# Optimization experiments

Measured on AMD Instinct MI355X. Metric: run time of the kernel, lower is better.

## Reference

```python
import jax, jax.numpy as jnp
import numpy as np

N, E = 50000, 600000
IN_DIM, HID, OUT = 512, 256, 64
NEG_SLOPE = 0.2  # pyg GATConv default negative_slope


def setup_inputs() -> dict:
    key = jax.random.key(0)
    ks = jax.random.split(key, 6)
    features = jax.random.normal(ks[0], (N, IN_DIM), jnp.float32)
    edge_index = jax.random.randint(ks[1], (2, E), 0, N)
    W1 = jax.random.normal(ks[2], (IN_DIM, HID), jnp.float32) * (1.0 / np.sqrt(IN_DIM))
    W2 = jax.random.normal(ks[3], (HID, OUT), jnp.float32) * (1.0 / np.sqrt(HID))
    att_src = jax.random.normal(ks[4], (HID,), jnp.float32) * 0.1
    att_dst = jax.random.normal(ks[5], (HID,), jnp.float32) * 0.1
    return {"features": features, "W1": W1, "W2": W2,
            "att_src": att_src, "att_dst": att_dst, "edge_index": edge_index}


def _gat_propagate(h_pre, a_src, a_dst, src, dst, n):
    """STAGATE GATConv message passing (heads=1, concat=False, no self loops).

    Per-edge logit = leaky_relu(alpha_src[src] + alpha_dst[dst]),
    softmax over edges sharing the same dst, scatter-add of weighted src feats.
    """
    logits = jax.nn.leaky_relu(a_src[src] + a_dst[dst], NEG_SLOPE)        # [E]
    m = jax.ops.segment_max(logits, dst, num_segments=n)                   # [N]
    ex = jnp.exp(logits - m[dst])                                          # [E]
    denom = jax.ops.segment_sum(ex, dst, num_segments=n)                   # [N]
    w = ex / (denom[dst] + 1e-16)                                          # [E], pyg softmax eps
    return jax.ops.segment_sum(h_pre[src] * w[:, None], dst, num_segments=n)  # [N, C]


def reference(features, W1, W2, att_src, att_dst, edge_index):
    src, dst = edge_index[0], edge_index[1]
    n = features.shape[0]
    # conv1: attention computed and cached (self.attentions)
    hp1 = features @ W1                      # [N, HID]
    a_s = hp1 @ att_src                      # [N] per-node src attention score
    a_d = hp1 @ att_dst                      # [N] per-node dst attention score
    h1 = jax.nn.elu(_gat_propagate(hp1, a_s, a_d, src, dst, n))
    # conv2: attention=False -> plain linear
    h2 = h1 @ W2                             # [N, OUT]
    # conv3: weights = conv2.lin_src.T, tied_attention = conv1.attentions
    hp3 = h2 @ W2.T                          # [N, HID]
    h3 = jax.nn.elu(_gat_propagate(hp3, a_s, a_d, src, dst, n))
    # conv4: weights = conv1.lin_src.T, attention=False
    h4 = h3 @ W1.T                           # [N, IN_DIM]
    return (h2, h4)
```

## Files before the change

kernel.cpp:

```cpp
#include <hip/hip_runtime.h>
#include <hip/hip_bf16.h>
#include <cstdint>
#include <cstddef>

#define IN_DIM 512
#define HID 256
#define OUTD 64
#define NEG_SLOPE 0.2f

typedef __attribute__((ext_vector_type(8))) __bf16 bfrag_t;
typedef __attribute__((ext_vector_type(4))) float facc_t;
typedef __attribute__((ext_vector_type(4))) unsigned int u32x4;

__device__ __forceinline__ float bf2f(unsigned short u) {
  return __uint_as_float(((unsigned int)u) << 16);
}
__device__ __forceinline__ unsigned short f2bf(float f) {
  unsigned int x = __float_as_uint(f);
  x = (x + 0x7FFFu + ((x >> 16) & 1u)) >> 16;
  return (unsigned short)x;
}

#define GLOAD_LDS16(g, l)                                              \
  __builtin_amdgcn_global_load_lds(                                    \
      (const __attribute__((address_space(1))) void*)(g),              \
      (__attribute__((address_space(3))) void*)(l), 16, 0, 0)

template <int BM, int BN>
__global__ __launch_bounds__(256) void gemm_bt(const unsigned short* __restrict__ A,
                                               const unsigned short* __restrict__ B,
                                               void* __restrict__ Craw,
                                               unsigned short* __restrict__ Cb,
                                               int M, int N, int K, int c32, int act) {
  constexpr int FM = BM / 32, FN = BN / 32;
  constexpr int RT = BM + BN;
  __shared__ __align__(16) unsigned short lds[RT * 32];

  const int bm0 = blockIdx.x * BM;
  const int bn0 = blockIdx.y * BN;
  const int tid = threadIdx.x;
  const int lane = tid & 63;
  const int wave = tid >> 6;
  const int wrow = (wave >> 1) * (BM / 2);
  const int wcol = (wave & 1) * (BN / 2);
  const int lr = lane & 15;
  const int quad = lane >> 4;
  const int swz = (quad ^ (lr & 3)) << 3;

  facc_t acc[FM][FN];
#pragma unroll
  for (int i = 0; i < FM; ++i)
#pragma unroll
    for (int j = 0; j < FN; ++j) acc[i][j] = (facc_t){0.f, 0.f, 0.f, 0.f};

  for (int k0 = 0; k0 < K; k0 += 32) {
    __syncthreads();
#pragma unroll
    for (int t = wave; t < RT / 16; t += 4) {
      const int r0 = t * 16;
      const int row = r0 + (lane >> 2);
      const int seg = (lane & 3) ^ (row & 3);
      const unsigned short* g;
      if (r0 < BM) {
        int gm = bm0 + row;
        if (gm >= M) gm = M - 1;
        g = A + (size_t)gm * K + k0 + seg * 8;
      } else {
        g = B + (size_t)(bn0 + row - BM) * K + k0 + seg * 8;
      }
      GLOAD_LDS16(g, lds + t * 512);
    }
    __syncthreads();

    bfrag_t a[FM], b[FN];
#pragma unroll
    for (int i = 0; i < FM; ++i)
      a[i] = *(const bfrag_t*)&lds[(wrow + i * 16 + lr) * 32 + swz];
#pragma unroll
    for (int j = 0; j < FN; ++j)
      b[j] = *(const bfrag_t*)&lds[(BM + wcol + j * 16 + lr) * 32 + swz];
#pragma unroll
    for (int i = 0; i < FM; ++i)
#pragma unroll
      for (int j = 0; j < FN; ++j)
        acc[i][j] = __builtin_amdgcn_mfma_f32_16x16x32_bf16(a[i], b[j], acc[i][j], 0, 0, 0);
  }

#pragma unroll
  for (int i = 0; i < FM; ++i)
#pragma unroll
    for (int r = 0; r < 4; ++r) {
      const int grow = bm0 + wrow + i * 16 + quad * 4 + r;
      if (grow < M) {
#pragma unroll
        for (int j = 0; j < FN; ++j) {
          const int gcol = bn0 + wcol + j * 16 + lr;
          float v = acc[i][j][r];
          if (act) v = v > 0.f ? v : (expf(v) - 1.f);
          if (c32) ((float*)Craw)[(size_t)grow * N + gcol] = v;
          else ((unsigned short*)Craw)[(size_t)grow * N + gcol] = f2bf(v);
          if (Cb) Cb[(size_t)grow * N + gcol] = f2bf(v);
        }
      }
    }
}

template <int BM, int BN>
__global__ __launch_bounds__(256) void gemm_a32_bt(const float* __restrict__ A,
                                                   const unsigned short* __restrict__ B,
                                                   unsigned short* __restrict__ C,
                                                   int M, int N, int K) {
  constexpr int FM = BM / 32, FN = BN / 32;
  constexpr int RT = BM + BN;
  __shared__ __align__(16) unsigned short lds[RT * 32];

  const int bm0 = blockIdx.x * BM;
  const int bn0 = blockIdx.y * BN;
  const int tid = threadIdx.x;
  const int lane = tid & 63;
  const int wave = tid >> 6;
  const int wrow = (wave >> 1) * (BM / 2);
  const int wcol = (wave & 1) * (BN / 2);
  const int lr = lane & 15;
  const int quad = lane >> 4;
  const int swz = (quad ^ (lr & 3)) << 3;

  const int arow0 = tid >> 2;
  const int aseg = tid & 3;

  facc_t acc[FM][FN];
#pragma unroll
  for (int i = 0; i < FM; ++i)
#pragma unroll
    for (int j = 0; j < FN; ++j) acc[i][j] = (facc_t){0.f, 0.f, 0.f, 0.f};

  for (int k0 = 0; k0 < K; k0 += 32) {
    __syncthreads();
#pragma unroll
    for (int t = wave; t < BN / 16; t += 4) {
      const int lr0 = BM + t * 16;
      const int row = lr0 + (lane >> 2);
      const int seg = (lane & 3) ^ (row & 3);
      const unsigned short* g = B + (size_t)(bn0 + t * 16 + (lane >> 2)) * K + k0 + seg * 8;
      GLOAD_LDS16(g, lds + lr0 * 32);
    }
#pragma unroll
    for (int h = 0; h < 2; ++h) {
      const int row = arow0 + h * (BM / 2);
      int gm = bm0 + row;
      if (gm >= M) gm = M - 1;
      const float* g = A + (size_t)gm * K + k0 + aseg * 8;
      const float4 fa = ((const float4*)g)[0];
      const float4 fb = ((const float4*)g)[1];
      u32x4 pk;
      pk.x = (unsigned int)f2bf(fa.x) | ((unsigned int)f2bf(fa.y) << 16);
      pk.y = (unsigned int)f2bf(fa.z) | ((unsigned int)f2bf(fa.w) << 16);
      pk.z = (unsigned int)f2bf(fb.x) | ((unsigned int)f2bf(fb.y) << 16);
      pk.w = (unsigned int)f2bf(fb.z) | ((unsigned int)f2bf(fb.w) << 16);
      *(u32x4*)&lds[row * 32 + ((aseg ^ (row & 3)) << 3)] = pk;
    }
    __syncthreads();

    bfrag_t a[FM], b[FN];
#pragma unroll
    for (int i = 0; i < FM; ++i)
      a[i] = *(const bfrag_t*)&lds[(wrow + i * 16 + lr) * 32 + swz];
#pragma unroll
    for (int j = 0; j < FN; ++j)
      b[j] = *(const bfrag_t*)&lds[(BM + wcol + j * 16 + lr) * 32 + swz];
#pragma unroll
    for (int i = 0; i < FM; ++i)
#pragma unroll
      for (int j = 0; j < FN; ++j)
        acc[i][j] = __builtin_amdgcn_mfma_f32_16x16x32_bf16(a[i], b[j], acc[i][j], 0, 0, 0);
  }

#pragma unroll
  for (int i = 0; i < FM; ++i)
#pragma unroll
    for (int r = 0; r < 4; ++r) {
      const int grow = bm0 + wrow + i * 16 + quad * 4 + r;
      if (grow < M) {
#pragma unroll
        for (int j = 0; j < FN; ++j) {
          const int gcol = bn0 + wcol + j * 16 + lr;
          C[(size_t)grow * N + gcol] = f2bf(acc[i][j][r]);
        }
      }
    }
}

__global__ void cvt_weights(const float* __restrict__ W1, const float* __restrict__ W2,
                            unsigned short* __restrict__ W1T, unsigned short* __restrict__ W1b,
                            unsigned short* __restrict__ W2T, unsigned short* __restrict__ W2b) {
  const int idx = blockIdx.x * 256 + threadIdx.x;
  if (idx < IN_DIM * HID) {
    const unsigned short b = f2bf(W1[idx]);
    W1b[idx] = b;
    const int r = idx >> 8, c = idx & 255;
    W1T[(size_t)c * IN_DIM + r] = b;
  }
  if (idx < HID * OUTD) {
    const unsigned short b = f2bf(W2[idx]);
    W2b[idx] = b;
    const int r = idx >> 6, c = idx & 63;
    W2T[(size_t)c * HID + r] = b;
  }
}

__global__ __launch_bounds__(256) void rowdot(const unsigned short* __restrict__ hp,
                                              const float* __restrict__ att_s,
                                              const float* __restrict__ att_d,
                                              float* __restrict__ as_, float* __restrict__ ad_,
                                              int n) {
  const int node = blockIdx.x * 4 + (threadIdx.x >> 6);
  if (node >= n) return;
  const int lane = threadIdx.x & 63;
  const unsigned short* row = hp + (size_t)node * HID + (lane << 2);
  float s = 0.f, d = 0.f;
#pragma unroll
  for (int j = 0; j < 4; ++j) {
    const float h = bf2f(row[j]);
    s += h * att_s[(lane << 2) + j];
    d += h * att_d[(lane << 2) + j];
  }
  for (int off = 32; off > 0; off >>= 1) {
    s += __shfl_down(s, off);
    d += __shfl_down(d, off);
  }
  if (lane == 0) { as_[node] = s; ad_[node] = d; }
}

__global__ void init_deg(int* __restrict__ deg, int n) {
  const int i = blockIdx.x * 256 + threadIdx.x;
  if (i < n) deg[i] = 0;
}

__global__ void edge_pass1(const int* __restrict__ src, const int* __restrict__ dst,
                           const float* __restrict__ as_, const float* __restrict__ ad_,
                           float* __restrict__ eexp, int* __restrict__ deg, int E, int n) {
  const int e = blockIdx.x * 256 + threadIdx.x;
  if (e >= E) return;
  const int s = src[e], d = dst[e];
  if ((unsigned)s >= (unsigned)n || (unsigned)d >= (unsigned)n) return;
  float l = as_[s] + ad_[d];
  l = l > 0.f ? l : NEG_SLOPE * l;
  eexp[e] = expf(fminf(l, 60.f));
  atomicAdd(&deg[d], 1);
}

__global__ __launch_bounds__(256) void scan_reduce(const int* __restrict__ deg,
                                                   int* __restrict__ bsum, int n) {
  __shared__ int ws4[4];
  const int tid = threadIdx.x, lane = tid & 63, wid = tid >> 6;
  const int base = blockIdx.x * 2048 + tid * 8;
  int s = 0;
#pragma unroll
  for (int j = 0; j < 8; ++j) {
    const int i = base + j;
    if (i < n) s += deg[i];
  }
  for (int off = 32; off > 0; off >>= 1) s += __shfl_down(s, off);
  if (lane == 0) ws4[wid] = s;
  __syncthreads();
  if (tid == 0) bsum[blockIdx.x] = ws4[0] + ws4[1] + ws4[2] + ws4[3];
}

__global__ __launch_bounds__(256) void scan_final(const int* __restrict__ deg,
                                                  const int* __restrict__ bsum,
                                                  int* __restrict__ row_ptr,
                                                  int* __restrict__ cursor, int n) {
  __shared__ int wsum[4];
  __shared__ int blockoff;
  const int tid = threadIdx.x, lane = tid & 63, wid = tid >> 6;
  if (wid == 0) {
    int v = (lane < blockIdx.x) ? bsum[lane] : 0;
    for (int off = 32; off > 0; off >>= 1) v += __shfl_down(v, off);
    if (lane == 0) blockoff = v;
  }
  const int base = blockIdx.x * 2048 + tid * 8;
  int v[8], s = 0;
#pragma unroll
  for (int j = 0; j < 8; ++j) {
    const int i = base + j;
    v[j] = (i < n) ? deg[i] : 0;
    s += v[j];
  }
  int ws = s;
  for (int off = 1; off < 64; off <<= 1) {
    const int t = __shfl_up(ws, off);
    if (lane >= off) ws += t;
  }
  if (lane == 63) wsum[wid] = ws;
  __syncthreads();
  int woff = 0;
  for (int w_ = 0; w_ < wid; ++w_) woff += wsum[w_];
  int run = blockoff + woff + (ws - s);
#pragma unroll
  for (int j = 0; j < 8; ++j) {
    const int i = base + j;
    if (i < n) {
      cursor[i] = run;
      row_ptr[i + 1] = run + v[j];
    }
    run += v[j];
  }
  if (blockIdx.x == 0 && tid == 0) row_ptr[0] = 0;
}

__global__ void edge_scatter(const int* __restrict__ src, const int* __restrict__ dst,
                             const float* __restrict__ eexp, int* __restrict__ cursor,
                             int2* __restrict__ csr, int E, int n) {
  const int e = blockIdx.x * 256 + threadIdx.x;
  if (e >= E) return;
  const int s = src[e], d = dst[e];
  if ((unsigned)s >= (unsigned)n || (unsigned)d >= (unsigned)n) return;
  const int pos = atomicAdd(&cursor[d], 1);
  int2 c;
  c.x = s;
  c.y = __float_as_int(eexp[e]);
  csr[pos] = c;
}

__global__ __launch_bounds__(256) void gat_prop256(const unsigned short* __restrict__ hpre,
                                                   const int* __restrict__ row_ptr,
                                                   const int2* __restrict__ csr,
                                                   unsigned short* __restrict__ out, int n) {
  const int node = blockIdx.x * 4 + (threadIdx.x >> 6);
  if (node >= n) return;
  const int lane = threadIdx.x & 63;
  const int half = lane >> 5;
  const int lh = lane & 31;
  const int beg = row_ptr[node], end = row_ptr[node + 1];
  const unsigned short* base = hpre + (lh << 3);
  float a[8] = {0.f, 0.f, 0.f, 0.f, 0.f, 0.f, 0.f, 0.f};
  float wsum = 0.f;
  int e = beg;
  for (; e + 8 <= end; e += 8) {
#pragma unroll
    for (int u = 0; u < 4; ++u) {
      const int2 c = csr[e + 2 * u + half];
      const float w = __int_as_float(c.y);
      const u32x4 v = *(const u32x4*)(base + (size_t)c.x * HID);
      wsum += w;
      a[0] += w * bf2f((unsigned short)(v.x & 0xffffu));
      a[1] += w * bf2f((unsigned short)(v.x >> 16));
      a[2] += w * bf2f((unsigned short)(v.y & 0xffffu));
      a[3] += w * bf2f((unsigned short)(v.y >> 16));
      a[4] += w * bf2f((unsigned short)(v.z & 0xffffu));
      a[5] += w * bf2f((unsigned short)(v.z >> 16));
      a[6] += w * bf2f((unsigned short)(v.w & 0xffffu));
      a[7] += w * bf2f((unsigned short)(v.w >> 16));
    }
  }
  for (; e < end; e += 2) {
    const int e2 = e + half;
    if (e2 < end) {
      const int2 c = csr[e2];
      const float w = __int_as_float(c.y);
      const u32x4 v = *(const u32x4*)(base + (size_t)c.x * HID);
      wsum += w;
      a[0] += w * bf2f((unsigned short)(v.x & 0xffffu));
      a[1] += w * bf2f((unsigned short)(v.x >> 16));
      a[2] += w * bf2f((unsigned short)(v.y & 0xffffu));
      a[3] += w * bf2f((unsigned short)(v.y >> 16));
      a[4] += w * bf2f((unsigned short)(v.z & 0xffffu));
      a[5] += w * bf2f((unsigned short)(v.z >> 16));
      a[6] += w * bf2f((unsigned short)(v.w & 0xffffu));
      a[7] += w * bf2f((unsigned short)(v.w >> 16));
    }
  }
#pragma unroll
  for (int i = 0; i < 8; ++i) a[i] += __shfl_xor(a[i], 32);
  wsum += __shfl_xor(wsum, 32);
  if (half == 0) {
    const float inv = 1.f / (wsum + 1e-16f);
#pragma unroll
    for (int i = 0; i < 8; ++i) {
      a[i] *= inv;
      a[i] = a[i] > 0.f ? a[i] : (expf(a[i]) - 1.f);
    }
    u32x4 o;
    o.x = (unsigned int)f2bf(a[0]) | ((unsigned int)f2bf(a[1]) << 16);
    o.y = (unsigned int)f2bf(a[2]) | ((unsigned int)f2bf(a[3]) << 16);
    o.z = (unsigned int)f2bf(a[4]) | ((unsigned int)f2bf(a[5]) << 16);
    o.w = (unsigned int)f2bf(a[6]) | ((unsigned int)f2bf(a[7]) << 16);
    *(u32x4*)(out + (size_t)node * HID + (lh << 3)) = o;
  }
}

__global__ __launch_bounds__(256) void gat_prop64(const unsigned short* __restrict__ hpre,
                                                  const int* __restrict__ row_ptr,
                                                  const int2* __restrict__ csr,
                                                  unsigned short* __restrict__ out, int n) {
  const int node = blockIdx.x * 4 + (threadIdx.x >> 6);
  if (node >= n) return;
  const int lane = threadIdx.x & 63;
  const int quad = lane >> 4;
  const int lr = lane & 15;
  const int beg = row_ptr[node], end = row_ptr[node + 1];
  const unsigned short* base = hpre + (lr << 2);
  float a0 = 0.f, a1 = 0.f, a2 = 0.f, a3 = 0.f, wsum = 0.f;
  int e = beg;
  for (; e + 8 <= end; e += 8) {
#pragma unroll
    for (int u = 0; u < 2; ++u) {
      const int2 c = csr[e + 4 * u + quad];
      const float w = __int_as_float(c.y);
      const uint2 v = *(const uint2*)(base + (size_t)c.x * OUTD);
      wsum += w;
      a0 += w * bf2f((unsigned short)(v.x & 0xffffu));
      a1 += w * bf2f((unsigned short)(v.x >> 16));
      a2 += w * bf2f((unsigned short)(v.y & 0xffffu));
      a3 += w * bf2f((unsigned short)(v.y >> 16));
    }
  }
  for (; e < end; e += 4) {
    const int e2 = e + quad;
    if (e2 < end) {
      const int2 c = csr[e2];
      const float w = __int_as_float(c.y);
      const uint2 v = *(const uint2*)(base + (size_t)c.x * OUTD);
      wsum += w;
      a0 += w * bf2f((unsigned short)(v.x & 0xffffu));
      a1 += w * bf2f((unsigned short)(v.x >> 16));
      a2 += w * bf2f((unsigned short)(v.y & 0xffffu));
      a3 += w * bf2f((unsigned short)(v.y >> 16));
    }
  }
  a0 += __shfl_xor(a0, 16); a0 += __shfl_xor(a0, 32);
  a1 += __shfl_xor(a1, 16); a1 += __shfl_xor(a1, 32);
  a2 += __shfl_xor(a2, 16); a2 += __shfl_xor(a2, 32);
  a3 += __shfl_xor(a3, 16); a3 += __shfl_xor(a3, 32);
  wsum += __shfl_xor(wsum, 16); wsum += __shfl_xor(wsum, 32);
  if (quad == 0) {
    const float inv = 1.f / (wsum + 1e-16f);
    uint2 o;
    o.x = (unsigned int)f2bf(a0 * inv) | ((unsigned int)f2bf(a1 * inv) << 16);
    o.y = (unsigned int)f2bf(a2 * inv) | ((unsigned int)f2bf(a3 * inv) << 16);
    *(uint2*)(out + (size_t)node * OUTD + (lr << 2)) = o;
  }
}

extern "C" void kernel_launch(void* const* d_in, const int* in_sizes, int n_in,
                              void* d_out, int out_size, void* d_ws, size_t ws_size,
                              hipStream_t stream) {
  const float* feat = (const float*)d_in[0];
  const float* W1 = (const float*)d_in[1];
  const float* W2 = (const float*)d_in[2];
  const float* att_s = (const float*)d_in[3];
  const float* att_d = (const float*)d_in[4];
  const int* ei = (const int*)d_in[5];
  const int N = in_sizes[0] / IN_DIM;
  const int E = in_sizes[5] / 2;
  const int* src = ei;
  const int* dst = ei + E;
  float* outf = (float*)d_out;

  unsigned short* hp1 = (unsigned short*)(outf + (size_t)N * OUTD);
  unsigned short* g2 = hp1 + (size_t)N * HID;

  char* w = (char*)d_ws;
  size_t off = 0;
  auto alloc = [&](size_t bytes) -> void* {
    void* p = w + off;
    off += (bytes + 255) & ~(size_t)255;
    return p;
  };
  unsigned short* h1h3 = (unsigned short*)alloc((size_t)N * HID * 2);
  unsigned short* h2b = (unsigned short*)alloc((size_t)N * OUTD * 2);
  float* a_src_v = (float*)alloc((size_t)N * 4);
  float* a_dst_v = (float*)alloc((size_t)N * 4);
  float* eexp = (float*)alloc((size_t)E * 4);
  int* deg = (int*)alloc((size_t)N * 4);
  int* row_ptr = (int*)alloc((size_t)(N + 1) * 4);
  int* cursor = (int*)alloc((size_t)N * 4);
  int* bsum = (int*)alloc((size_t)64 * 4);
  int2* csr = (int2*)alloc((size_t)E * 8);
  unsigned short* W1T = (unsigned short*)alloc((size_t)IN_DIM * HID * 2);
  unsigned short* W1b = (unsigned short*)alloc((size_t)IN_DIM * HID * 2);
  unsigned short* W2T = (unsigned short*)alloc((size_t)HID * OUTD * 2);
  unsigned short* W2b = (unsigned short*)alloc((size_t)HID * OUTD * 2);

  const int EB = (E + 255) / 256;
  const int NB = (N + 255) / 256;
  const int MB = (N + 127) / 128;
  const int SB = (N + 2047) / 2048;

  cvt_weights<<<(IN_DIM * HID + 255) / 256, 256, 0, stream>>>(W1, W2, W1T, W1b, W2T, W2b);

  gemm_a32_bt<128, 128><<<dim3(MB, HID / 128), 256, 0, stream>>>(feat, W1T, hp1,
                                                                 N, HID, IN_DIM);
  rowdot<<<(N + 3) / 4, 256, 0, stream>>>(hp1, att_s, att_d, a_src_v, a_dst_v, N);

  init_deg<<<NB, 256, 0, stream>>>(deg, N);
  edge_pass1<<<EB, 256, 0, stream>>>(src, dst, a_src_v, a_dst_v, eexp, deg, E, N);
  scan_reduce<<<SB, 256, 0, stream>>>(deg, bsum, N);
  scan_final<<<SB, 256, 0, stream>>>(deg, bsum, row_ptr, cursor, N);
  edge_scatter<<<EB, 256, 0, stream>>>(src, dst, eexp, cursor, csr, E, N);

  gat_prop256<<<(N + 3) / 4, 256, 0, stream>>>(hp1, row_ptr, csr, h1h3, N);
  gemm_bt<128, 64><<<dim3(MB, OUTD / 64), 256, 0, stream>>>(h1h3, W2T, outf, h2b,
                                                            N, OUTD, HID, 1, 0);
  gat_prop64<<<(N + 3) / 4, 256, 0, stream>>>(h2b, row_ptr, csr, g2, N);
  gemm_bt<128, 128><<<dim3(MB, HID / 128), 256, 0, stream>>>(g2, W2b, h1h3, nullptr,
                                                             N, HID, OUTD, 0, 1);
  gemm_bt<128, 128><<<dim3(MB, IN_DIM / 128), 256, 0, stream>>>(h1h3, W1b,
                                                                outf + (size_t)N * OUTD,
                                                                nullptr, N, IN_DIM, HID, 1, 0);
}
```

Before: 451.4 us.

## Fuse attention row-dots into first GEMM, batch CSR loads via shuffles, widen GEMM tiles

The first GEMM now covers the full 256-column output per block and computes the per-node src/dst attention dot products in its epilogue, so the separate rowdot kernel and its re-read of hp1 go away. Both GAT propagation kernels load up to 64 CSR entries per node in a single coalesced read and broadcast them with wave shuffles, instead of issuing a dependent load per edge. The later GEMMs switch to 128x256 tiles. The wider tiles mean more accumulator registers and LDS per block, which may lower occupancy and leave fewer blocks in the grid.

Result: slower. 503.1 us (+11.5%).

```diff
diff --git a/kernel.cpp b/kernel.cpp
--- a/kernel.cpp
+++ b/kernel.cpp
@@ -106,16 +106,19 @@
 }
 
 template <int BM, int BN>
-__global__ __launch_bounds__(256) void gemm_a32_bt(const float* __restrict__ A,
-                                                   const unsigned short* __restrict__ B,
-                                                   unsigned short* __restrict__ C,
-                                                   int M, int N, int K) {
+__global__ __launch_bounds__(256) void gemm_a32_bt_att(const float* __restrict__ A,
+                                                       const unsigned short* __restrict__ B,
+                                                       unsigned short* __restrict__ C,
+                                                       const float* __restrict__ att_s,
+                                                       const float* __restrict__ att_d,
+                                                       float* __restrict__ as_,
+                                                       float* __restrict__ ad_,
+                                                       int M, int N, int K) {
   constexpr int FM = BM / 32, FN = BN / 32;
   constexpr int RT = BM + BN;
   __shared__ __align__(16) unsigned short lds[RT * 32];
 
   const int bm0 = blockIdx.x * BM;
-  const int bn0 = blockIdx.y * BN;
   const int tid = threadIdx.x;
   const int lane = tid & 63;
   const int wave = tid >> 6;
@@ -141,7 +144,7 @@
       const int lr0 = BM + t * 16;
       const int row = lr0 + (lane >> 2);
       const int seg = (lane & 3) ^ (row & 3);
-      const unsigned short* g = B + (size_t)(bn0 + t * 16 + (lane >> 2)) * K + k0 + seg * 8;
+      const unsigned short* g = B + (size_t)(t * 16 + (lane >> 2)) * K + k0 + seg * 8;
       GLOAD_LDS16(g, lds + lr0 * 32);
     }
 #pragma unroll
@@ -175,19 +178,47 @@
         acc[i][j] = __builtin_amdgcn_mfma_f32_16x16x32_bf16(a[i], b[j], acc[i][j], 0, 0, 0);
   }
 
+  float av_s[FN], av_d[FN];
+#pragma unroll
+  for (int j = 0; j < FN; ++j) {
+    av_s[j] = att_s[wcol + j * 16 + lr];
+    av_d[j] = att_d[wcol + j * 16 + lr];
+  }
+  float* redS = (float*)lds;
+  float* redD = (float*)lds + 2 * BM;
+  __syncthreads();
+
 #pragma unroll
   for (int i = 0; i < FM; ++i)
 #pragma unroll
     for (int r = 0; r < 4; ++r) {
       const int grow = bm0 + wrow + i * 16 + quad * 4 + r;
-      if (grow < M) {
-#pragma unroll
-        for (int j = 0; j < FN; ++j) {
-          const int gcol = bn0 + wcol + j * 16 + lr;
-          C[(size_t)grow * N + gcol] = f2bf(acc[i][j][r]);
-        }
+      float ps = 0.f, pd = 0.f;
+#pragma unroll
+      for (int j = 0; j < FN; ++j) {
+        const float v = acc[i][j][r];
+        ps += v * av_s[j];
+        pd += v * av_d[j];
+        if (grow < M) C[(size_t)grow * N + (wcol + j * 16 + lr)] = f2bf(v);
       }
-    }
+      ps += __shfl_xor(ps, 1); ps += __shfl_xor(ps, 2);
+      ps += __shfl_xor(ps, 4); ps += __shfl_xor(ps, 8);
+      pd += __shfl_xor(pd, 1); pd += __shfl_xor(pd, 2);
+      pd += __shfl_xor(pd, 4); pd += __shfl_xor(pd, 8);
+      if (lr == 0) {
+        const int rloc = wrow + i * 16 + quad * 4 + r;
+        redS[(wave & 1) * BM + rloc] = ps;
+        redD[(wave & 1) * BM + rloc] = pd;
+      }
+    }
+  __syncthreads();
+  if (tid < BM) {
+    const int grow = bm0 + tid;
+    if (grow < M) {
+      as_[grow] = redS[tid] + redS[BM + tid];
+      ad_[grow] = redD[tid] + redD[BM + tid];
+    }
+  }
 }
 
 __global__ void cvt_weights(const float* __restrict__ W1, const float* __restrict__ W2,
@@ -206,29 +237,6 @@
     const int r = idx >> 6, c = idx & 63;
     W2T[(size_t)c * HID + r] = b;
   }
-}
-
-__global__ __launch_bounds__(256) void rowdot(const unsigned short* __restrict__ hp,
-                                              const float* __restrict__ att_s,
-                                              const float* __restrict__ att_d,
-                                              float* __restrict__ as_, float* __restrict__ ad_,
-                                              int n) {
-  const int node = blockIdx.x * 4 + (threadIdx.x >> 6);
-  if (node >= n) return;
-  const int lane = threadIdx.x & 63;
-  const unsigned short* row = hp + (size_t)node * HID + (lane << 2);
-  float s = 0.f, d = 0.f;
-#pragma unroll
-  for (int j = 0; j < 4; ++j) {
-    const float h = bf2f(row[j]);
-    s += h * att_s[(lane << 2) + j];
-    d += h * att_d[(lane << 2) + j];
-  }
-  for (int off = 32; off > 0; off >>= 1) {
-    s += __shfl_down(s, off);
-    d += __shfl_down(d, off);
-  }
-  if (lane == 0) { as_[node] = s; ad_[node] = d; }
 }
 
 __global__ void init_deg(int* __restrict__ deg, int n) {
@@ -332,16 +340,29 @@
   const int half = lane >> 5;
   const int lh = lane & 31;
   const int beg = row_ptr[node], end = row_ptr[node + 1];
+  const int deg = end - beg;
   const unsigned short* base = hpre + (lh << 3);
   float a[8] = {0.f, 0.f, 0.f, 0.f, 0.f, 0.f, 0.f, 0.f};
   float wsum = 0.f;
-  int e = beg;
-  for (; e + 8 <= end; e += 8) {
-#pragma unroll
-    for (int u = 0; u < 4; ++u) {
-      const int2 c = csr[e + 2 * u + half];
-      const float w = __int_as_float(c.y);
-      const u32x4 v = *(const u32x4*)(base + (size_t)c.x * HID);
+
+  int cs = 0;
+  float cw = 0.f;
+  if (lane < deg) {
+    const int2 t = csr[beg + lane];
+    cs = t.x;
+    cw = __int_as_float(t.y);
+  }
+  const int dmain = deg < 64 ? deg : 64;
+  for (int j0 = 0; j0 < dmain; j0 += 16) {
+#pragma unroll
+    for (int u = 0; u < 8; ++u) {
+      const int j = j0 + 2 * u + half;
+      const bool valid = j < dmain;
+      const int jj = valid ? j : 0;
+      const int s = __shfl(cs, jj);
+      float w = __shfl(cw, jj);
+      w = valid ? w : 0.f;
+      const u32x4 v = *(const u32x4*)(base + (size_t)s * HID);
       wsum += w;
       a[0] += w * bf2f((unsigned short)(v.x & 0xffffu));
       a[1] += w * bf2f((unsigned short)(v.x >> 16));
@@ -353,7 +374,7 @@
       a[7] += w * bf2f((unsigned short)(v.w >> 16));
     }
   }
-  for (; e < end; e += 2) {
+  for (int e = beg + 64; e < end; e += 2) {
     const int e2 = e + half;
     if (e2 < end) {
       const int2 c = csr[e2];
@@ -399,15 +420,28 @@
   const int quad = lane >> 4;
   const int lr = lane & 15;
   const int beg = row_ptr[node], end = row_ptr[node + 1];
+  const int deg = end - beg;
   const unsigned short* base = hpre + (lr << 2);
   float a0 = 0.f, a1 = 0.f, a2 = 0.f, a3 = 0.f, wsum = 0.f;
-  int e = beg;
-  for (; e + 8 <= end; e += 8) {
-#pragma unroll
-    for (int u = 0; u < 2; ++u) {
-      const int2 c = csr[e + 4 * u + quad];
-      const float w = __int_as_float(c.y);
-      const uint2 v = *(const uint2*)(base + (size_t)c.x * OUTD);
+
+  int cs = 0;
+  float cw = 0.f;
+  if (lane < deg) {
+    const int2 t = csr[beg + lane];
+    cs = t.x;
+    cw = __int_as_float(t.y);
+  }
+  const int dmain = deg < 64 ? deg : 64;
+  for (int j0 = 0; j0 < dmain; j0 += 16) {
+#pragma unroll
+    for (int u = 0; u < 4; ++u) {
+      const int j = j0 + 4 * u + quad;
+      const bool valid = j < dmain;
+      const int jj = valid ? j : 0;
+      const int s = __shfl(cs, jj);
+      float w = __shfl(cw, jj);
+      w = valid ? w : 0.f;
+      const uint2 v = *(const uint2*)(base + (size_t)s * OUTD);
       wsum += w;
       a0 += w * bf2f((unsigned short)(v.x & 0xffffu));
       a1 += w * bf2f((unsigned short)(v.x >> 16));
@@ -415,7 +449,7 @@
       a3 += w * bf2f((unsigned short)(v.y >> 16));
     }
   }
-  for (; e < end; e += 4) {
+  for (int e = beg + 64; e < end; e += 4) {
     const int e2 = e + quad;
     if (e2 < end) {
       const int2 c = csr[e2];
@@ -489,9 +523,8 @@
 
   cvt_weights<<<(IN_DIM * HID + 255) / 256, 256, 0, stream>>>(W1, W2, W1T, W1b, W2T, W2b);
 
-  gemm_a32_bt<128, 128><<<dim3(MB, HID / 128), 256, 0, stream>>>(feat, W1T, hp1,
-                                                                 N, HID, IN_DIM);
-  rowdot<<<(N + 3) / 4, 256, 0, stream>>>(hp1, att_s, att_d, a_src_v, a_dst_v, N);
+  gemm_a32_bt_att<128, 256><<<MB, 256, 0, stream>>>(feat, W1T, hp1, att_s, att_d,
+                                                    a_src_v, a_dst_v, N, HID, IN_DIM);
 
   init_deg<<<NB, 256, 0, stream>>>(deg, N);
   edge_pass1<<<EB, 256, 0, stream>>>(src, dst, a_src_v, a_dst_v, eexp, deg, E, N);
@@ -503,9 +536,9 @@
   gemm_bt<128, 64><<<dim3(MB, OUTD / 64), 256, 0, stream>>>(h1h3, W2T, outf, h2b,
                                                             N, OUTD, HID, 1, 0);
   gat_prop64<<<(N + 3) / 4, 256, 0, stream>>>(h2b, row_ptr, csr, g2, N);
-  gemm_bt<128, 128><<<dim3(MB, HID / 128), 256, 0, stream>>>(g2, W2b, h1h3, nullptr,
+  gemm_bt<128, 256><<<dim3(MB, HID / 256), 256, 0, stream>>>(g2, W2b, h1h3, nullptr,
                                                              N, HID, OUTD, 0, 1);
-  gemm_bt<128, 128><<<dim3(MB, IN_DIM / 128), 256, 0, stream>>>(h1h3, W1b,
+  gemm_bt<128, 256><<<dim3(MB, IN_DIM / 256), 256, 0, stream>>>(h1h3, W1b,
                                                                 outf + (size_t)N * OUTD,
                                                                 nullptr, N, IN_DIM, HID, 1, 0);
 }
```
